# Performance work log

Measured on AMD Instinct MI355X. Metric: run time of the kernel, lower is better.

Reference implementation:

```python
import jax, jax.numpy as jnp
import numpy as np

UNIT_NO, T_DIM, K_DIM, H_DIM, P_DIM, F_DIM = 512, 25, 20, 64, 4096, 10
BATCH = 32


def setup_inputs() -> dict:
    key = jax.random.key(0)
    ks = jax.random.split(key, 9)
    S = jax.random.normal(ks[0], (BATCH, UNIT_NO * T_DIM), dtype=jnp.float32)
    pix_units = jax.random.randint(ks[1], (P_DIM, K_DIM), 0, UNIT_NO)
    # per-unit featurize Linear(t_dim -> f_dim)
    Wf = jax.random.normal(ks[2], (UNIT_NO, T_DIM, F_DIM), dtype=jnp.float32) / np.sqrt(T_DIM)
    bf = jax.random.normal(ks[3], (UNIT_NO, F_DIM), dtype=jnp.float32) * 0.01
    # per-pixel hidden Linear(k_dim*f_dim -> h_dim)
    W1 = jax.random.normal(ks[4], (P_DIM, K_DIM * F_DIM, H_DIM), dtype=jnp.float32) / np.sqrt(K_DIM * F_DIM)
    b1 = jax.random.normal(ks[5], (P_DIM, H_DIM), dtype=jnp.float32) * 0.01
    # per-pixel PReLU slope (nn.PReLU() default: single param, init 0.25)
    a = jnp.full((P_DIM,), 0.25, dtype=jnp.float32)
    # per-pixel output Linear(h_dim -> 1)
    Wo = jax.random.normal(ks[6], (P_DIM, H_DIM), dtype=jnp.float32) / np.sqrt(H_DIM)
    bo = jax.random.normal(ks[7], (P_DIM,), dtype=jnp.float32) * 0.01
    return {"S": S, "pix_units": pix_units, "Wf": Wf, "bf": bf,
            "W1": W1, "b1": b1, "a": a, "Wo": Wo, "bo": bo}


def reference(S, pix_units, Wf, bf, W1, b1, a, Wo, bo):
    B = S.shape[0]
    # per-unit featurize: [B, unit_no, t_dim] x [unit_no, t_dim, f_dim] -> [B, unit_no, f_dim]
    Sn = S.reshape(B, UNIT_NO, T_DIM)
    F = jnp.einsum('bnt,ntf->bnf', Sn, Wf) + bf  # [B, N, f]
    # gather k units per pixel and concat their features: [B, p, k, f] -> [B, p, k*f]
    G = F[:, pix_units].reshape(B, P_DIM, K_DIM * F_DIM)
    # per-pixel hidden layer + PReLU
    H = jnp.einsum('bpk,pkh->bph', G, W1) + b1  # [B, p, h]
    H = jnp.where(H >= 0, H, a[None, :, None] * H)
    # per-pixel scalar output
    I = jnp.einsum('bph,ph->bp', H, Wo) + bo  # [B, p]
    return I
```

## Files before the change

### kernel.cpp

```cpp
#include <hip/hip_runtime.h>
#include <hip/hip_bf16.h>

#define UNIT_NO 512
#define T_DIM 25
#define K_DIM 20
#define H_DIM 64
#define P_DIM 4096
#define F_DIM 10
#define BATCH 32
#define KTOT (K_DIM * F_DIM)
#define KPAD 224
#define LSTR 232
#define FTB_STR 16

typedef short bf16x8 __attribute__((ext_vector_type(8)));
typedef float f32x4 __attribute__((ext_vector_type(4)));

__device__ inline unsigned short bf16b(float x) {
    __hip_bfloat16 h = __float2bfloat16(x);
    return *(unsigned short*)&h;
}
__device__ inline unsigned int pack2(float lo, float hi) {
    return (unsigned int)bf16b(lo) | ((unsigned int)bf16b(hi) << 16);
}

__global__ __launch_bounds__(320) void featurize_kernel(
    const float* __restrict__ S, const float* __restrict__ Wf,
    const float* __restrict__ bf, unsigned short* __restrict__ Ftb)
{
    const int u = blockIdx.x;
    __shared__ float Ws[T_DIM * F_DIM];
    __shared__ float Ss[BATCH * T_DIM];
    const int tid = threadIdx.x;
    for (int i = tid; i < T_DIM * F_DIM; i += 320)
        Ws[i] = Wf[u * (T_DIM * F_DIM) + i];
    for (int i = tid; i < BATCH * T_DIM; i += 320) {
        int b = i / T_DIM;
        int t = i - b * T_DIM;
        Ss[i] = S[b * (UNIT_NO * T_DIM) + u * T_DIM + t];
    }
    if (tid < 192) {
        int b  = tid / 6;
        int fz = 10 + (tid - b * 6);
        Ftb[(u * BATCH + b) * FTB_STR + fz] = 0;
    }
    __syncthreads();
    const int b = tid / F_DIM;
    const int f = tid - b * F_DIM;
    float acc = 0.f;
#pragma unroll
    for (int t = 0; t < T_DIM; ++t)
        acc = fmaf(Ss[b * T_DIM + t], Ws[t * F_DIM + f], acc);
    Ftb[(u * BATCH + b) * FTB_STR + f] = bf16b(acc + bf[u * F_DIM + f]);
}

__global__ __launch_bounds__(256, 5) void pixel_fast_kernel(
    const unsigned short* __restrict__ Ftb, const int* __restrict__ pix_units,
    const float* __restrict__ W1, const float* __restrict__ b1,
    const float* __restrict__ a, const float* __restrict__ Wo,
    const float* __restrict__ bo, float* __restrict__ out)
{
    const int p = blockIdx.x;
    const int tid = threadIdx.x;
    const int lane = tid & 63;
    const int wv = tid >> 6;
    const int l16 = lane & 15;
    const int l4  = lane >> 4;

    __shared__ unsigned short Gb[BATCH][LSTR];
    __shared__ float red[4][BATCH];

    const float* __restrict__ w1p =
        W1 + (size_t)p * (KTOT * H_DIM) + (wv << 4) + l16;
    const int krow = 8 * l4;

    uint4 ga[3]; unsigned int gb2[3];
#pragma unroll
    for (int it = 0; it < 3; ++it) {
        const int task = tid + it * 256;
        if (it < 2 || tid < (K_DIM * BATCH - 512)) {
            const int b = task & 31;
            const int u = pix_units[p * K_DIM + (task >> 5)];
            const unsigned short* __restrict__ src =
                Ftb + ((size_t)(u * BATCH + b) * FTB_STR);
            ga[it]  = *(const uint4*)(src);
            gb2[it] = *(const unsigned int*)(src + 8);
        }
    }

    if (tid < BATCH * 6) {
        const int row = tid / 6;
        const int c   = tid - row * 6;
        *(uint2*)(&Gb[row][KTOT + (c << 2)]) = make_uint2(0u, 0u);
    }
#pragma unroll
    for (int it = 0; it < 3; ++it) {
        const int task = tid + it * 256;
        if (it < 2 || tid < (K_DIM * BATCH - 512)) {
            const int j = task >> 5;
            const int b = task & 31;
            unsigned int* dst = (unsigned int*)(&Gb[b][j * F_DIM]);
            dst[0] = ga[it].x;
            dst[1] = ga[it].y;
            dst[2] = ga[it].z;
            dst[3] = ga[it].w;
            dst[4] = gb2[it];
        }
    }

    float wf0[4][8];
#pragma unroll
    for (int kt = 0; kt < 4; ++kt)
#pragma unroll
        for (int j = 0; j < 8; ++j)
            wf0[kt][j] = w1p[(size_t)(32 * kt + krow + j) * H_DIM];

    float wf1[3][8];
#pragma unroll
    for (int kt2 = 0; kt2 < 3; ++kt2) {
        const int kt = 4 + kt2;
#pragma unroll
        for (int j = 0; j < 8; ++j) {
            const int k = 32 * kt + krow + j;
            wf1[kt2][j] = (k < KTOT) ? w1p[(size_t)k * H_DIM] : 0.f;
        }
    }

    bf16x8 bfrag[7];
#pragma unroll
    for (int kt = 0; kt < 4; ++kt) {
        union { bf16x8 v; unsigned int u[4]; } t_;
        t_.u[0] = pack2(wf0[kt][0], wf0[kt][1]);
        t_.u[1] = pack2(wf0[kt][2], wf0[kt][3]);
        t_.u[2] = pack2(wf0[kt][4], wf0[kt][5]);
        t_.u[3] = pack2(wf0[kt][6], wf0[kt][7]);
        bfrag[kt] = t_.v;
    }

#pragma unroll
    for (int kt2 = 0; kt2 < 3; ++kt2) {
        union { bf16x8 v; unsigned int u[4]; } t_;
        t_.u[0] = pack2(wf1[kt2][0], wf1[kt2][1]);
        t_.u[1] = pack2(wf1[kt2][2], wf1[kt2][3]);
        t_.u[2] = pack2(wf1[kt2][4], wf1[kt2][5]);
        t_.u[3] = pack2(wf1[kt2][6], wf1[kt2][7]);
        bfrag[4 + kt2] = t_.v;
    }
    __syncthreads();

    f32x4 acc0 = {0.f, 0.f, 0.f, 0.f};
    f32x4 acc1 = {0.f, 0.f, 0.f, 0.f};
    const unsigned short* __restrict__ Arow0 = &Gb[l16][krow];
    const unsigned short* __restrict__ Arow1 = &Gb[16 + l16][krow];
#pragma unroll
    for (int kt = 0; kt < KPAD / 32; ++kt) {
        bf16x8 fa0 = *(const bf16x8*)(Arow0 + kt * 32);
        bf16x8 fa1 = *(const bf16x8*)(Arow1 + kt * 32);
        acc0 = __builtin_amdgcn_mfma_f32_16x16x32_bf16(fa0, bfrag[kt], acc0, 0, 0, 0);
        acc1 = __builtin_amdgcn_mfma_f32_16x16x32_bf16(fa1, bfrag[kt], acc1, 0, 0, 0);
    }

    const int h = (wv << 4) + l16;
    const float b1v = b1[p * H_DIM + h];
    const float wov = Wo[p * H_DIM + h];
    const float av  = a[p];
    float s0[4], s1[4];
#pragma unroll
    for (int r = 0; r < 4; ++r) {
        float v0 = acc0[r] + b1v; v0 = (v0 >= 0.f) ? v0 : av * v0;
        float v1 = acc1[r] + b1v; v1 = (v1 >= 0.f) ? v1 : av * v1;
        s0[r] = v0 * wov;
        s1[r] = v1 * wov;
    }
#pragma unroll
    for (int off = 1; off < 16; off <<= 1)
#pragma unroll
        for (int r = 0; r < 4; ++r) {
            s0[r] += __shfl_xor(s0[r], off);
            s1[r] += __shfl_xor(s1[r], off);
        }
    if (l16 == 0) {
#pragma unroll
        for (int r = 0; r < 4; ++r) {
            red[wv][(l4 << 2) + r]      = s0[r];
            red[wv][16 + (l4 << 2) + r] = s1[r];
        }
    }
    __syncthreads();
    if (tid < BATCH) {
        float v = red[0][tid] + red[1][tid] + red[2][tid] + red[3][tid] + bo[p];
        out[(size_t)tid * P_DIM + p] = v;
    }
}

__global__ __launch_bounds__(256, 3) void pixel_safe_kernel(
    const unsigned short* __restrict__ Ftb, const int* __restrict__ pix_units,
    const float* __restrict__ W1, const float* __restrict__ b1,
    const float* __restrict__ a, const float* __restrict__ Wo,
    const float* __restrict__ bo, float* __restrict__ out,
    const float* __restrict__ S, const float* __restrict__ Wf,
    const float* __restrict__ bf, int Ustar)
{
    const int p = blockIdx.x;
    const int tid = threadIdx.x;
    const int lane = tid & 63;
    const int wv = tid >> 6;
    const int l16 = lane & 15;
    const int l4  = lane >> 4;

    __shared__ unsigned short Gb[BATCH][LSTR];
    __shared__ float red[4][BATCH];

    const float* __restrict__ w1p =
        W1 + (size_t)p * (KTOT * H_DIM) + (wv << 4) + l16;
    const int krow = 8 * l4;

    uint4 ga[3]; unsigned int gb2[3];
#pragma unroll
    for (int it = 0; it < 3; ++it) {
        int task = tid + it * 256;
        if (task < K_DIM * BATCH) {
            const int b = task & 31;
            const int u = pix_units[p * K_DIM + (task >> 5)];
            if (u < Ustar) {
                const unsigned short* __restrict__ src =
                    Ftb + ((size_t)(u * BATCH + b) * FTB_STR);
                ga[it]  = *(const uint4*)(src);
                gb2[it] = *(const unsigned int*)(src + 8);
            } else {
                const float* __restrict__ sp = S + b * (UNIT_NO * T_DIM) + u * T_DIM;
                const float* __restrict__ wp = Wf + u * (T_DIM * F_DIM);
                float g[10];
#pragma unroll
                for (int ff = 0; ff < F_DIM; ++ff) {
                    float acc = bf[u * F_DIM + ff];
#pragma unroll
                    for (int t = 0; t < T_DIM; ++t)
                        acc = fmaf(sp[t], wp[t * F_DIM + ff], acc);
                    g[ff] = acc;
                }
                ga[it].x = pack2(g[0], g[1]);
                ga[it].y = pack2(g[2], g[3]);
                ga[it].z = pack2(g[4], g[5]);
                ga[it].w = pack2(g[6], g[7]);
                gb2[it]  = pack2(g[8], g[9]);
            }
        }
    }
    if (tid < BATCH * 6) {
        const int row = tid / 6;
        const int c   = tid - row * 6;
        *(uint2*)(&Gb[row][KTOT + (c << 2)]) = make_uint2(0u, 0u);
    }
#pragma unroll
    for (int it = 0; it < 3; ++it) {
        int task = tid + it * 256;
        if (task < K_DIM * BATCH) {
            const int j = task >> 5;
            const int b = task & 31;
            unsigned int* dst = (unsigned int*)(&Gb[b][j * F_DIM]);
            dst[0] = ga[it].x; dst[1] = ga[it].y; dst[2] = ga[it].z;
            dst[3] = ga[it].w; dst[4] = gb2[it];
        }
    }

    bf16x8 bfrag[7];
#pragma unroll
    for (int kt = 0; kt < 7; ++kt) {
        float wf[8];
#pragma unroll
        for (int j = 0; j < 8; ++j) {
            const int k = 32 * kt + krow + j;
            wf[j] = (k < KTOT) ? w1p[(size_t)k * H_DIM] : 0.f;
        }
        union { bf16x8 v; unsigned int u[4]; } t_;
        t_.u[0] = pack2(wf[0], wf[1]);
        t_.u[1] = pack2(wf[2], wf[3]);
        t_.u[2] = pack2(wf[4], wf[5]);
        t_.u[3] = pack2(wf[6], wf[7]);
        bfrag[kt] = t_.v;
    }
    __syncthreads();

    f32x4 acc0 = {0.f, 0.f, 0.f, 0.f};
    f32x4 acc1 = {0.f, 0.f, 0.f, 0.f};
    const unsigned short* __restrict__ Arow0 = &Gb[l16][krow];
    const unsigned short* __restrict__ Arow1 = &Gb[16 + l16][krow];
#pragma unroll
    for (int kt = 0; kt < KPAD / 32; ++kt) {
        bf16x8 fa0 = *(const bf16x8*)(Arow0 + kt * 32);
        bf16x8 fa1 = *(const bf16x8*)(Arow1 + kt * 32);
        acc0 = __builtin_amdgcn_mfma_f32_16x16x32_bf16(fa0, bfrag[kt], acc0, 0, 0, 0);
        acc1 = __builtin_amdgcn_mfma_f32_16x16x32_bf16(fa1, bfrag[kt], acc1, 0, 0, 0);
    }

    const int h = (wv << 4) + l16;
    const float b1v = b1[p * H_DIM + h];
    const float wov = Wo[p * H_DIM + h];
    const float av  = a[p];
    float s0[4], s1[4];
#pragma unroll
    for (int r = 0; r < 4; ++r) {
        float v0 = acc0[r] + b1v; v0 = (v0 >= 0.f) ? v0 : av * v0;
        float v1 = acc1[r] + b1v; v1 = (v1 >= 0.f) ? v1 : av * v1;
        s0[r] = v0 * wov;
        s1[r] = v1 * wov;
    }
#pragma unroll
    for (int off = 1; off < 16; off <<= 1)
#pragma unroll
        for (int r = 0; r < 4; ++r) {
            s0[r] += __shfl_xor(s0[r], off);
            s1[r] += __shfl_xor(s1[r], off);
        }
    if (l16 == 0) {
#pragma unroll
        for (int r = 0; r < 4; ++r) {
            red[wv][(l4 << 2) + r]      = s0[r];
            red[wv][16 + (l4 << 2) + r] = s1[r];
        }
    }
    __syncthreads();
    if (tid < BATCH) {
        float v = red[0][tid] + red[1][tid] + red[2][tid] + red[3][tid] + bo[p];
        out[(size_t)tid * P_DIM + p] = v;
    }
}

extern "C" void kernel_launch(void* const* d_in, const int* in_sizes, int n_in,
                              void* d_out, int out_size, void* d_ws, size_t ws_size,
                              hipStream_t stream) {
    const float* S         = (const float*)d_in[0];
    const int*   pix_units = (const int*)d_in[1];
    const float* Wf        = (const float*)d_in[2];
    const float* bf        = (const float*)d_in[3];
    const float* W1        = (const float*)d_in[4];
    const float* b1        = (const float*)d_in[5];
    const float* a         = (const float*)d_in[6];
    const float* Wo        = (const float*)d_in[7];
    const float* bo        = (const float*)d_in[8];
    float* out = (float*)d_out;
    unsigned short* Ftb = (unsigned short*)d_ws;

    int Ustar = (int)(ws_size / (size_t)(BATCH * FTB_STR * sizeof(unsigned short)));
    if (Ustar > UNIT_NO) Ustar = UNIT_NO;

    if (Ustar > 0)
        featurize_kernel<<<Ustar, 320, 0, stream>>>(S, Wf, bf, Ftb);

    if (Ustar >= UNIT_NO) {
        pixel_fast_kernel<<<P_DIM, 256, 0, stream>>>(Ftb, pix_units, W1, b1, a,
                                                     Wo, bo, out);
    } else {
        pixel_safe_kernel<<<P_DIM, 256, 0, stream>>>(Ftb, pix_units, W1, b1, a,
                                                     Wo, bo, out, S, Wf, bf, Ustar);
    }
}
```

Before: 46.18 us.

## Process two pixels per block to overlap second pixel's weight loads with MFMA

The fast pixel kernel now handles two pixels per block. It gathers both feature tiles up front and issues the W1 loads for the second pixel before running the first pixel's MFMA and epilogue, so memory latency overlaps with compute. The aim is more memory-level parallelism per wave in this bandwidth-bound W1 stream. In exchange, register pressure and LDS use per block rise, the occupancy hint drops from 5 to 4, and the grid is halved.

```diff
diff --git a/kernel.cpp b/kernel.cpp
--- a/kernel.cpp
+++ b/kernel.cpp
@@ -54,142 +54,233 @@
     Ftb[(u * BATCH + b) * FTB_STR + f] = bf16b(acc + bf[u * F_DIM + f]);
 }
 
-__global__ __launch_bounds__(256, 5) void pixel_fast_kernel(
+#define GATHER_PIXEL(pp, ga, gb2)                                             \
+    _Pragma("unroll")                                                         \
+    for (int it = 0; it < 3; ++it) {                                          \
+        const int task = tid + it * 256;                                      \
+        if (it < 2 || tid < (K_DIM * BATCH - 512)) {                          \
+            const int b = task & 31;                                          \
+            const int u = pix_units[(pp) * K_DIM + (task >> 5)];              \
+            const unsigned short* __restrict__ src =                          \
+                Ftb + ((size_t)(u * BATCH + b) * FTB_STR);                    \
+            ga[it]  = *(const uint4*)(src);                                   \
+            gb2[it] = *(const unsigned int*)(src + 8);                        \
+        }                                                                     \
+    }
+
+#define WRITE_GB(Gb, ga, gb2)                                                 \
+    if (tid < BATCH * 6) {                                                    \
+        const int row = tid / 6;                                              \
+        const int c   = tid - row * 6;                                        \
+        *(uint2*)(&Gb[row][KTOT + (c << 2)]) = make_uint2(0u, 0u);            \
+    }                                                                         \
+    _Pragma("unroll")                                                         \
+    for (int it = 0; it < 3; ++it) {                                          \
+        const int task = tid + it * 256;                                      \
+        if (it < 2 || tid < (K_DIM * BATCH - 512)) {                          \
+            const int j = task >> 5;                                          \
+            const int b = task & 31;                                          \
+            unsigned int* dst = (unsigned int*)(&Gb[b][j * F_DIM]);           \
+            dst[0] = ga[it].x; dst[1] = ga[it].y; dst[2] = ga[it].z;          \
+            dst[3] = ga[it].w; dst[4] = gb2[it];                              \
+        }                                                                     \
+    }
+
+__global__ __launch_bounds__(256, 4) void pixel_fast2_kernel(
     const unsigned short* __restrict__ Ftb, const int* __restrict__ pix_units,
     const float* __restrict__ W1, const float* __restrict__ b1,
     const float* __restrict__ a, const float* __restrict__ Wo,
     const float* __restrict__ bo, float* __restrict__ out)
 {
-    const int p = blockIdx.x;
+    const int pA = blockIdx.x << 1;
+    const int pB = pA + 1;
     const int tid = threadIdx.x;
     const int lane = tid & 63;
     const int wv = tid >> 6;
     const int l16 = lane & 15;
     const int l4  = lane >> 4;
 
-    __shared__ unsigned short Gb[BATCH][LSTR];
-    __shared__ float red[4][BATCH];
-
-    const float* __restrict__ w1p =
-        W1 + (size_t)p * (KTOT * H_DIM) + (wv << 4) + l16;
+    __shared__ unsigned short GbA[BATCH][LSTR];
+    __shared__ unsigned short GbB[BATCH][LSTR];
+    __shared__ float redA[4][BATCH];
+    __shared__ float redB[4][BATCH];
+
     const int krow = 8 * l4;
-
-    uint4 ga[3]; unsigned int gb2[3];
-#pragma unroll
-    for (int it = 0; it < 3; ++it) {
-        const int task = tid + it * 256;
-        if (it < 2 || tid < (K_DIM * BATCH - 512)) {
-            const int b = task & 31;
-            const int u = pix_units[p * K_DIM + (task >> 5)];
-            const unsigned short* __restrict__ src =
-                Ftb + ((size_t)(u * BATCH + b) * FTB_STR);
-            ga[it]  = *(const uint4*)(src);
-            gb2[it] = *(const unsigned int*)(src + 8);
-        }
-    }
-
-    if (tid < BATCH * 6) {
-        const int row = tid / 6;
-        const int c   = tid - row * 6;
-        *(uint2*)(&Gb[row][KTOT + (c << 2)]) = make_uint2(0u, 0u);
-    }
-#pragma unroll
-    for (int it = 0; it < 3; ++it) {
-        const int task = tid + it * 256;
-        if (it < 2 || tid < (K_DIM * BATCH - 512)) {
-            const int j = task >> 5;
-            const int b = task & 31;
-            unsigned int* dst = (unsigned int*)(&Gb[b][j * F_DIM]);
-            dst[0] = ga[it].x;
-            dst[1] = ga[it].y;
-            dst[2] = ga[it].z;
-            dst[3] = ga[it].w;
-            dst[4] = gb2[it];
-        }
-    }
-
-    float wf0[4][8];
+    const float* __restrict__ w1pA =
+        W1 + (size_t)pA * (KTOT * H_DIM) + (wv << 4) + l16;
+    const float* __restrict__ w1pB =
+        W1 + (size_t)pB * (KTOT * H_DIM) + (wv << 4) + l16;
+
+    uint4 gaA[3]; unsigned int gb2A[3];
+    uint4 gaB[3]; unsigned int gb2B[3];
+    GATHER_PIXEL(pA, gaA, gb2A)
+    GATHER_PIXEL(pB, gaB, gb2B)
+    WRITE_GB(GbA, gaA, gb2A)
+    WRITE_GB(GbB, gaB, gb2B)
+
+    float wfA0[4][8];
 #pragma unroll
     for (int kt = 0; kt < 4; ++kt)
 #pragma unroll
         for (int j = 0; j < 8; ++j)
-            wf0[kt][j] = w1p[(size_t)(32 * kt + krow + j) * H_DIM];
-
-    float wf1[3][8];
+            wfA0[kt][j] = w1pA[(size_t)(32 * kt + krow + j) * H_DIM];
+    float wfA1[3][8];
 #pragma unroll
     for (int kt2 = 0; kt2 < 3; ++kt2) {
         const int kt = 4 + kt2;
 #pragma unroll
         for (int j = 0; j < 8; ++j) {
             const int k = 32 * kt + krow + j;
-            wf1[kt2][j] = (k < KTOT) ? w1p[(size_t)k * H_DIM] : 0.f;
-        }
-    }
-
-    bf16x8 bfrag[7];
+            wfA1[kt2][j] = (k < KTOT) ? w1pA[(size_t)k * H_DIM] : 0.f;
+        }
+    }
+
+    bf16x8 bfragA[7];
 #pragma unroll
     for (int kt = 0; kt < 4; ++kt) {
         union { bf16x8 v; unsigned int u[4]; } t_;
-        t_.u[0] = pack2(wf0[kt][0], wf0[kt][1]);
-        t_.u[1] = pack2(wf0[kt][2], wf0[kt][3]);
-        t_.u[2] = pack2(wf0[kt][4], wf0[kt][5]);
-        t_.u[3] = pack2(wf0[kt][6], wf0[kt][7]);
-        bfrag[kt] = t_.v;
-    }
-
+        t_.u[0] = pack2(wfA0[kt][0], wfA0[kt][1]);
+        t_.u[1] = pack2(wfA0[kt][2], wfA0[kt][3]);
+        t_.u[2] = pack2(wfA0[kt][4], wfA0[kt][5]);
+        t_.u[3] = pack2(wfA0[kt][6], wfA0[kt][7]);
+        bfragA[kt] = t_.v;
+    }
 #pragma unroll
     for (int kt2 = 0; kt2 < 3; ++kt2) {
         union { bf16x8 v; unsigned int u[4]; } t_;
-        t_.u[0] = pack2(wf1[kt2][0], wf1[kt2][1]);
-        t_.u[1] = pack2(wf1[kt2][2], wf1[kt2][3]);
-        t_.u[2] = pack2(wf1[kt2][4], wf1[kt2][5]);
-        t_.u[3] = pack2(wf1[kt2][6], wf1[kt2][7]);
-        bfrag[4 + kt2] = t_.v;
-    }
+        t_.u[0] = pack2(wfA1[kt2][0], wfA1[kt2][1]);
+        t_.u[1] = pack2(wfA1[kt2][2], wfA1[kt2][3]);
+        t_.u[2] = pack2(wfA1[kt2][4], wfA1[kt2][5]);
+        t_.u[3] = pack2(wfA1[kt2][6], wfA1[kt2][7]);
+        bfragA[4 + kt2] = t_.v;
+    }
+
+    __builtin_amdgcn_sched_barrier(0);
+    float wfB0[4][8];
+#pragma unroll
+    for (int kt = 0; kt < 4; ++kt)
+#pragma unroll
+        for (int j = 0; j < 8; ++j)
+            wfB0[kt][j] = w1pB[(size_t)(32 * kt + krow + j) * H_DIM];
+    float wfB1[3][8];
+#pragma unroll
+    for (int kt2 = 0; kt2 < 3; ++kt2) {
+        const int kt = 4 + kt2;
+#pragma unroll
+        for (int j = 0; j < 8; ++j) {
+            const int k = 32 * kt + krow + j;
+            wfB1[kt2][j] = (k < KTOT) ? w1pB[(size_t)k * H_DIM] : 0.f;
+        }
+    }
+
     __syncthreads();
 
-    f32x4 acc0 = {0.f, 0.f, 0.f, 0.f};
-    f32x4 acc1 = {0.f, 0.f, 0.f, 0.f};
-    const unsigned short* __restrict__ Arow0 = &Gb[l16][krow];
-    const unsigned short* __restrict__ Arow1 = &Gb[16 + l16][krow];
-#pragma unroll
-    for (int kt = 0; kt < KPAD / 32; ++kt) {
-        bf16x8 fa0 = *(const bf16x8*)(Arow0 + kt * 32);
-        bf16x8 fa1 = *(const bf16x8*)(Arow1 + kt * 32);
-        acc0 = __builtin_amdgcn_mfma_f32_16x16x32_bf16(fa0, bfrag[kt], acc0, 0, 0, 0);
-        acc1 = __builtin_amdgcn_mfma_f32_16x16x32_bf16(fa1, bfrag[kt], acc1, 0, 0, 0);
-    }
-
-    const int h = (wv << 4) + l16;
-    const float b1v = b1[p * H_DIM + h];
-    const float wov = Wo[p * H_DIM + h];
-    const float av  = a[p];
-    float s0[4], s1[4];
-#pragma unroll
-    for (int r = 0; r < 4; ++r) {
-        float v0 = acc0[r] + b1v; v0 = (v0 >= 0.f) ? v0 : av * v0;
-        float v1 = acc1[r] + b1v; v1 = (v1 >= 0.f) ? v1 : av * v1;
-        s0[r] = v0 * wov;
-        s1[r] = v1 * wov;
-    }
-#pragma unroll
-    for (int off = 1; off < 16; off <<= 1)
+    const unsigned short* __restrict__ ArowA0 = &GbA[l16][krow];
+    const unsigned short* __restrict__ ArowA1 = &GbA[16 + l16][krow];
+    {
+        f32x4 acc0 = {0.f, 0.f, 0.f, 0.f};
+        f32x4 acc1 = {0.f, 0.f, 0.f, 0.f};
+#pragma unroll
+        for (int kt = 0; kt < KPAD / 32; ++kt) {
+            bf16x8 fa0 = *(const bf16x8*)(ArowA0 + kt * 32);
+            bf16x8 fa1 = *(const bf16x8*)(ArowA1 + kt * 32);
+            acc0 = __builtin_amdgcn_mfma_f32_16x16x32_bf16(fa0, bfragA[kt], acc0, 0, 0, 0);
+            acc1 = __builtin_amdgcn_mfma_f32_16x16x32_bf16(fa1, bfragA[kt], acc1, 0, 0, 0);
+        }
+        const int h = (wv << 4) + l16;
+        const float b1v = b1[pA * H_DIM + h];
+        const float wov = Wo[pA * H_DIM + h];
+        const float av  = a[pA];
+        float s0[4], s1[4];
 #pragma unroll
         for (int r = 0; r < 4; ++r) {
-            s0[r] += __shfl_xor(s0[r], off);
-            s1[r] += __shfl_xor(s1[r], off);
-        }
-    if (l16 == 0) {
+            float v0 = acc0[r] + b1v; v0 = (v0 >= 0.f) ? v0 : av * v0;
+            float v1 = acc1[r] + b1v; v1 = (v1 >= 0.f) ? v1 : av * v1;
+            s0[r] = v0 * wov;
+            s1[r] = v1 * wov;
+        }
+#pragma unroll
+        for (int off = 1; off < 16; off <<= 1)
+#pragma unroll
+            for (int r = 0; r < 4; ++r) {
+                s0[r] += __shfl_xor(s0[r], off);
+                s1[r] += __shfl_xor(s1[r], off);
+            }
+        if (l16 == 0) {
+#pragma unroll
+            for (int r = 0; r < 4; ++r) {
+                redA[wv][(l4 << 2) + r]      = s0[r];
+                redA[wv][16 + (l4 << 2) + r] = s1[r];
+            }
+        }
+    }
+
+    bf16x8 bfragB[7];
+#pragma unroll
+    for (int kt = 0; kt < 4; ++kt) {
+        union { bf16x8 v; unsigned int u[4]; } t_;
+        t_.u[0] = pack2(wfB0[kt][0], wfB0[kt][1]);
+        t_.u[1] = pack2(wfB0[kt][2], wfB0[kt][3]);
+        t_.u[2] = pack2(wfB0[kt][4], wfB0[kt][5]);
+        t_.u[3] = pack2(wfB0[kt][6], wfB0[kt][7]);
+        bfragB[kt] = t_.v;
+    }
+#pragma unroll
+    for (int kt2 = 0; kt2 < 3; ++kt2) {
+        union { bf16x8 v; unsigned int u[4]; } t_;
+        t_.u[0] = pack2(wfB1[kt2][0], wfB1[kt2][1]);
+        t_.u[1] = pack2(wfB1[kt2][2], wfB1[kt2][3]);
+        t_.u[2] = pack2(wfB1[kt2][4], wfB1[kt2][5]);
+        t_.u[3] = pack2(wfB1[kt2][6], wfB1[kt2][7]);
+        bfragB[4 + kt2] = t_.v;
+    }
+
+    const unsigned short* __restrict__ ArowB0 = &GbB[l16][krow];
+    const unsigned short* __restrict__ ArowB1 = &GbB[16 + l16][krow];
+    {
+        f32x4 acc0 = {0.f, 0.f, 0.f, 0.f};
+        f32x4 acc1 = {0.f, 0.f, 0.f, 0.f};
+#pragma unroll
+        for (int kt = 0; kt < KPAD / 32; ++kt) {
+            bf16x8 fa0 = *(const bf16x8*)(ArowB0 + kt * 32);
+            bf16x8 fa1 = *(const bf16x8*)(ArowB1 + kt * 32);
+            acc0 = __builtin_amdgcn_mfma_f32_16x16x32_bf16(fa0, bfragB[kt], acc0, 0, 0, 0);
+            acc1 = __builtin_amdgcn_mfma_f32_16x16x32_bf16(fa1, bfragB[kt], acc1, 0, 0, 0);
+        }
+        const int h = (wv << 4) + l16;
+        const float b1v = b1[pB * H_DIM + h];
+        const float wov = Wo[pB * H_DIM + h];
+        const float av  = a[pB];
+        float s0[4], s1[4];
 #pragma unroll
         for (int r = 0; r < 4; ++r) {
-            red[wv][(l4 << 2) + r]      = s0[r];
-            red[wv][16 + (l4 << 2) + r] = s1[r];
-        }
-    }
+            float v0 = acc0[r] + b1v; v0 = (v0 >= 0.f) ? v0 : av * v0;
+            float v1 = acc1[r] + b1v; v1 = (v1 >= 0.f) ? v1 : av * v1;
+            s0[r] = v0 * wov;
+            s1[r] = v1 * wov;
+        }
+#pragma unroll
+        for (int off = 1; off < 16; off <<= 1)
+#pragma unroll
+            for (int r = 0; r < 4; ++r) {
+                s0[r] += __shfl_xor(s0[r], off);
+                s1[r] += __shfl_xor(s1[r], off);
+            }
+        if (l16 == 0) {
+#pragma unroll
+            for (int r = 0; r < 4; ++r) {
+                redB[wv][(l4 << 2) + r]      = s0[r];
+                redB[wv][16 + (l4 << 2) + r] = s1[r];
+            }
+        }
+    }
+
     __syncthreads();
     if (tid < BATCH) {
-        float v = red[0][tid] + red[1][tid] + red[2][tid] + red[3][tid] + bo[p];
-        out[(size_t)tid * P_DIM + p] = v;
+        float vA = redA[0][tid] + redA[1][tid] + redA[2][tid] + redA[3][tid] + bo[pA];
+        float vB = redB[0][tid] + redB[1][tid] + redB[2][tid] + redB[3][tid] + bo[pB];
+        out[(size_t)tid * P_DIM + pA] = vA;
+        out[(size_t)tid * P_DIM + pB] = vB;
     }
 }
 
@@ -349,8 +440,8 @@
         featurize_kernel<<<Ustar, 320, 0, stream>>>(S, Wf, bf, Ftb);
 
     if (Ustar >= UNIT_NO) {
-        pixel_fast_kernel<<<P_DIM, 256, 0, stream>>>(Ftb, pix_units, W1, b1, a,
-                                                     Wo, bo, out);
+        pixel_fast2_kernel<<<P_DIM / 2, 256, 0, stream>>>(Ftb, pix_units, W1, b1,
+                                                          a, Wo, bo, out);
     } else {
         pixel_safe_kernel<<<P_DIM, 256, 0, stream>>>(Ftb, pix_units, W1, b1, a,
                                                      Wo, bo, out, S, Wf, bf, Ustar);
```

New measurement: 74.20 us. 1.61x slower.
